# Performance work log

Measured on AMD Instinct MI355X. Metric: run time of the kernel, lower is better.

Reference implementation:

```python
import jax, jax.numpy as jnp
import numpy as np
import math

FEATURE_DIM = 1024
NUM_HEADS = 16
HEAD_SIZE = FEATURE_DIM // NUM_HEADS


def setup_inputs() -> dict:
    key = jax.random.key(0)
    ks = jax.random.split(key, 5)
    B, T, C = 4, 2048, FEATURE_DIM
    scale = 1.0 / math.sqrt(C)
    x = jax.random.normal(ks[0], (B, T, C), dtype=jnp.float32)
    # attention_proj: Linear(C, 3C) -> weight (3C, C), bias (3C,)
    W_qkv = jax.random.uniform(ks[1], (3 * C, C), jnp.float32, -scale, scale)
    b_qkv = jax.random.uniform(ks[2], (3 * C,), jnp.float32, -scale, scale)
    # final_proj: Linear(C, C)
    W_out = jax.random.uniform(ks[3], (C, C), jnp.float32, -scale, scale)
    b_out = jax.random.uniform(ks[4], (C,), jnp.float32, -scale, scale)
    return {"x": x, "W_qkv": W_qkv, "b_qkv": b_qkv, "W_out": W_out, "b_out": b_out}


def reference(x, W_qkv, b_qkv, W_out, b_out):
    B, T, C = x.shape
    H, hs = NUM_HEADS, HEAD_SIZE
    qkv = x @ W_qkv.T + b_qkv                     # (B, T, 3C)
    qkv = qkv.reshape(B, T, H, 3 * hs)            # per-head interleaved q|k|v
    q = qkv[..., :hs]                             # (B, T, H, hs)
    k = qkv[..., hs:2 * hs]
    v = qkv[..., 2 * hs:]
    att = jnp.einsum('bthd,bshd->bhts', q, k) / math.sqrt(hs)  # (B, H, T, T)
    att_prob = jax.nn.softmax(att, axis=-1)
    att_v = jnp.einsum('bhts,bshd->bthd', att_prob, v)         # (B, T, H, hs)
    att_v = att_v.reshape(B, T, C)
    return att_v @ W_out.T + b_out
```

## Files before the change

### kernel.cpp

```cpp
#include <hip/hip_runtime.h>
#include <hip/hip_bf16.h>


typedef unsigned short u16;
typedef short bf16x8 __attribute__((ext_vector_type(8)));
typedef float floatx4 __attribute__((ext_vector_type(4)));

#define BB 4
#define TT 2048
#define CC 1024
#define HH 16
#define CEXP 0.18033688f

#if __has_builtin(__builtin_amdgcn_exp2f)
#define EXP2(x) __builtin_amdgcn_exp2f(x)
#else
#define EXP2(x) exp2f(x)
#endif

__device__ __forceinline__ u16 f2bf(float f) {
    __hip_bfloat16 h = __float2bfloat16(f);
    u16 r; __builtin_memcpy(&r, &h, 2); return r;
}
__device__ __forceinline__ unsigned pkbf(float lo, float hi) {
    __hip_bfloat162 h2 = __float22bfloat162_rn(float2{lo, hi});
    unsigned r; __builtin_memcpy(&r, &h2, 4); return r;
}
__device__ __forceinline__ bf16x8 cvt8(const float* p) {
    floatx4 a = *(const floatx4*)p;
    floatx4 b = *(const floatx4*)(p + 4);
    bf16x8 r;
    r[0] = (short)f2bf(a[0]); r[1] = (short)f2bf(a[1]);
    r[2] = (short)f2bf(a[2]); r[3] = (short)f2bf(a[3]);
    r[4] = (short)f2bf(b[0]); r[5] = (short)f2bf(b[1]);
    r[6] = (short)f2bf(b[2]); r[7] = (short)f2bf(b[3]);
    return r;
}
__device__ __forceinline__ int sw8(int row, int slot) {
    return row * 64 + (((slot ^ (row & 7)) & 7) << 3);
}
__device__ __forceinline__ void gll16(const u16* g, u16* l) {
    __builtin_amdgcn_global_load_lds(
        (const __attribute__((address_space(1))) unsigned*)g,
        (__attribute__((address_space(3))) unsigned*)l, 16, 0, 0);
}

__device__ __forceinline__ void pl32swap(unsigned& a, unsigned& b) {
#if __has_builtin(__builtin_amdgcn_permlane32_swap)
    typedef unsigned u32x2 __attribute__((ext_vector_type(2)));
    u32x2 r = __builtin_amdgcn_permlane32_swap(a, b, false, false);
    a = r[0]; b = r[1];
#else
    const bool up = (threadIdx.x & 32) != 0;
    unsigned as = (unsigned)__shfl_xor((int)a, 32);
    unsigned bs = (unsigned)__shfl_xor((int)b, 32);
    unsigned na = up ? bs : a;
    unsigned nb = up ? b : as;
    a = na; b = nb;
#endif
}
__device__ __forceinline__ void pl16swap(unsigned& a, unsigned& b) {
#if __has_builtin(__builtin_amdgcn_permlane16_swap)
    typedef unsigned u32x2 __attribute__((ext_vector_type(2)));
    u32x2 r = __builtin_amdgcn_permlane16_swap(a, b, false, false);
    a = r[0]; b = r[1];
#else
    const bool up = (threadIdx.x & 16) != 0;
    unsigned as = (unsigned)__shfl_xor((int)a, 16);
    unsigned bs = (unsigned)__shfl_xor((int)b, 16);
    unsigned na = up ? bs : a;
    unsigned nb = up ? b : as;
    a = na; b = nb;
#endif
}

__global__ __launch_bounds__(256) void cvt_all(const float* __restrict__ x,
                                               const float* __restrict__ wq,
                                               const float* __restrict__ wo,
                                               u16* __restrict__ xb,
                                               u16* __restrict__ wqb,
                                               u16* __restrict__ wob) {
    const int nx8 = 8388608 / 8, nq8 = 3145728 / 8, no8 = 1048576 / 8;
    const int n8 = nx8 + nq8 + no8;
    for (int i = blockIdx.x * blockDim.x + threadIdx.x; i < n8;
         i += gridDim.x * blockDim.x) {
        const float* src;
        u16* dst;
        if (i < nx8)            { src = x  + (size_t)i * 8;          dst = xb  + (size_t)i * 8; }
        else if (i < nx8 + nq8) { size_t j = i - nx8; src = wq + j * 8; dst = wqb + j * 8; }
        else                    { size_t j = i - nx8 - nq8; src = wo + j * 8; dst = wob + j * 8; }
        floatx4 a = *(const floatx4*)src;
        floatx4 b = *(const floatx4*)(src + 4);
        union { bf16x8 v; unsigned u[4]; } r;
        r.u[0] = pkbf(a[0], a[1]); r.u[1] = pkbf(a[2], a[3]);
        r.u[2] = pkbf(b[0], b[1]); r.u[3] = pkbf(b[2], b[3]);
        *(bf16x8*)dst = r.v;
    }
}

template <int SCATTER, int QSLOT>
__global__ __launch_bounds__(256) void gemm_lds(const u16* __restrict__ Ab,
                                                const u16* __restrict__ Bb,
                                                const float* __restrict__ bias,
                                                void* __restrict__ Cv,
                                                int K, int N) {
    __shared__ u16 As[128 * 64];
    __shared__ u16 Bs[128 * 64];

    const int tid  = threadIdx.x;
    const int lane = tid & 63;
    const int wave = tid >> 6;
    const int quad = lane >> 4;
    const int l15  = lane & 15;
    const int wm   = (wave >> 1) * 64;
    const int wn   = (wave & 1) * 64;
    const int blockM = blockIdx.y * 128;
    const int blockN = blockIdx.x * 128;

    floatx4 acc[4][4];
#pragma unroll
    for (int i = 0; i < 4; i++)
#pragma unroll
        for (int j = 0; j < 4; j++) acc[i][j] = (floatx4){0.f, 0.f, 0.f, 0.f};

    const int lr = lane >> 3;
    const int scol = ((lane & 7) ^ (lr & 7)) * 8;

    for (int k0 = 0; k0 < K; k0 += 64) {
        __syncthreads();
#pragma unroll
        for (int i = 0; i < 4; i++) {
            const int c = wave * 4 + i;
            const int row = blockM + c * 8 + lr;
            const u16* src;
            if (QSLOT) {
                const int b = row >> 11, t = row & 2047, h = k0 >> 6;
                src = Ab + ((size_t)((b * HH + h) * TT + t)) * 192 + scol;
            } else {
                src = Ab + (size_t)row * K + k0 + scol;
            }
            gll16(src, &As[c * 512]);
        }
#pragma unroll
        for (int i = 0; i < 4; i++) {
            const int c = wave * 4 + i;
            const int row = blockN + c * 8 + lr;
            gll16(Bb + (size_t)row * K + k0 + scol, &Bs[c * 512]);
        }
        __syncthreads();

#pragma unroll
        for (int ks = 0; ks < 2; ks++) {
            const int slot = ks * 4 + quad;
            bf16x8 af[4], bfr[4];
#pragma unroll
            for (int mi = 0; mi < 4; mi++)
                af[mi] = *(const bf16x8*)&As[sw8(wm + mi * 16 + l15, slot)];
#pragma unroll
            for (int ni = 0; ni < 4; ni++)
                bfr[ni] = *(const bf16x8*)&Bs[sw8(wn + ni * 16 + l15, slot)];
#pragma unroll
            for (int mi = 0; mi < 4; mi++)
#pragma unroll
                for (int ni = 0; ni < 4; ni++)
                    acc[mi][ni] = __builtin_amdgcn_mfma_f32_16x16x32_bf16(
                        af[mi], bfr[ni], acc[mi][ni], 0, 0, 0);
        }
    }

#pragma unroll
    for (int ni = 0; ni < 4; ni++) {
        const int col = blockN + wn + ni * 16 + l15;
        const float bv = bias[col];
        if (SCATTER) {
            const int h = col / 192;
            const int r = col - h * 192;
            const float qs = (r < 64) ? CEXP : 1.0f;
            u16* C = (u16*)Cv;
#pragma unroll
            for (int mi = 0; mi < 4; mi++)
#pragma unroll
                for (int reg = 0; reg < 4; reg++) {
                    const int row = blockM + wm + mi * 16 + quad * 4 + reg;
                    const int b = row >> 11, t = row & 2047;
                    C[((size_t)((b * HH + h) * TT + t)) * 192 + r] =
                        f2bf((acc[mi][ni][reg] + bv) * qs);
                }
        } else {
            float* C = (float*)Cv;
#pragma unroll
            for (int mi = 0; mi < 4; mi++)
#pragma unroll
                for (int reg = 0; reg < 4; reg++) {
                    const int row = blockM + wm + mi * 16 + quad * 4 + reg;
                    C[(size_t)row * N + col] = acc[mi][ni][reg] + bv;
                }
        }
    }
}

template <int SCATTER, int QSLOT>
__global__ __launch_bounds__(256) void gemm_bt(const void* __restrict__ Av,
                                               const float* __restrict__ Bw,
                                               const float* __restrict__ bias,
                                               void* __restrict__ Cv,
                                               int K, int N) {
    __shared__ u16 As[128 * 64];
    __shared__ u16 Bs[128 * 64];

    const int tid  = threadIdx.x;
    const int lane = tid & 63;
    const int wave = tid >> 6;
    const int quad = lane >> 4;
    const int l15  = lane & 15;
    const int wm   = (wave >> 1) * 64;
    const int wn   = (wave & 1) * 64;
    const int blockM = blockIdx.y * 128;
    const int blockN = blockIdx.x * 128;

    floatx4 acc[4][4];
#pragma unroll
    for (int i = 0; i < 4; i++)
#pragma unroll
        for (int j = 0; j < 4; j++) acc[i][j] = (floatx4){0.f, 0.f, 0.f, 0.f};

    const int srow = lane >> 3;
    const int scol = (lane & 7) * 8;

    for (int k0 = 0; k0 < K; k0 += 64) {
        bf16x8 at[4], bt[4];
#pragma unroll
        for (int i = 0; i < 4; i++) {
            const int row = blockM + (i * 4 + wave) * 8 + srow;
            if (QSLOT) {
                const int b = row >> 11, t = row & 2047, h = k0 >> 6;
                at[i] = *(const bf16x8*)((const u16*)Av
                         + ((size_t)((b * HH + h) * TT + t)) * 192 + scol);
            } else {
                at[i] = cvt8((const float*)Av + (size_t)row * K + k0 + scol);
            }
        }
#pragma unroll
        for (int i = 0; i < 4; i++)
            bt[i] = cvt8(Bw + (size_t)(blockN + (i * 4 + wave) * 8 + srow) * K + k0 + scol);

        __syncthreads();
#pragma unroll
        for (int i = 0; i < 4; i++)
            *(bf16x8*)&As[sw8((i * 4 + wave) * 8 + srow, lane & 7)] = at[i];
#pragma unroll
        for (int i = 0; i < 4; i++)
            *(bf16x8*)&Bs[sw8((i * 4 + wave) * 8 + srow, lane & 7)] = bt[i];
        __syncthreads();

#pragma unroll
        for (int ks = 0; ks < 2; ks++) {
            const int slot = ks * 4 + quad;
            bf16x8 af[4], bfr[4];
#pragma unroll
            for (int mi = 0; mi < 4; mi++)
                af[mi] = *(const bf16x8*)&As[sw8(wm + mi * 16 + l15, slot)];
#pragma unroll
            for (int ni = 0; ni < 4; ni++)
                bfr[ni] = *(const bf16x8*)&Bs[sw8(wn + ni * 16 + l15, slot)];
#pragma unroll
            for (int mi = 0; mi < 4; mi++)
#pragma unroll
                for (int ni = 0; ni < 4; ni++)
                    acc[mi][ni] = __builtin_amdgcn_mfma_f32_16x16x32_bf16(
                        af[mi], bfr[ni], acc[mi][ni], 0, 0, 0);
        }
    }

#pragma unroll
    for (int ni = 0; ni < 4; ni++) {
        const int col = blockN + wn + ni * 16 + l15;
        const float bv = bias[col];
        if (SCATTER) {
            const int h = col / 192;
            const int r = col - h * 192;
            const float qs = (r < 64) ? CEXP : 1.0f;
            u16* C = (u16*)Cv;
#pragma unroll
            for (int mi = 0; mi < 4; mi++)
#pragma unroll
                for (int reg = 0; reg < 4; reg++) {
                    const int row = blockM + wm + mi * 16 + quad * 4 + reg;
                    const int b = row >> 11, t = row & 2047;
                    C[((size_t)((b * HH + h) * TT + t)) * 192 + r] =
                        f2bf((acc[mi][ni][reg] + bv) * qs);
                }
        } else {
            float* C = (float*)Cv;
#pragma unroll
            for (int mi = 0; mi < 4; mi++)
#pragma unroll
                for (int reg = 0; reg < 4; reg++) {
                    const int row = blockM + wm + mi * 16 + quad * 4 + reg;
                    C[(size_t)row * N + col] = acc[mi][ni][reg] + bv;
                }
        }
    }
}

__global__ __launch_bounds__(256) void attn_fwd(u16* __restrict__ qkv) {
    __shared__ u16 Ks[64 * 64];
    __shared__ u16 Vts[64 * 64];

    const int tid  = threadIdx.x;
    const int lane = tid & 63;
    const int wave = tid >> 6;
    const int quad = lane >> 4;
    const int l15  = lane & 15;

    const int bh = blockIdx.y;
    const int t0 = blockIdx.x * 128;
    u16* Qg = qkv + (size_t)bh * TT * 192;

    bf16x8 qf[2][2];
#pragma unroll
    for (int qi = 0; qi < 2; qi++) {
        const int trow = t0 + wave * 32 + qi * 16 + l15;
#pragma unroll
        for (int ks = 0; ks < 2; ks++)
            qf[qi][ks] = *(const bf16x8*)(Qg + (size_t)trow * 192 + ks * 32 + quad * 8);
    }

    bf16x8 ones;
#pragma unroll
    for (int j = 0; j < 8; j++) ones[j] = (short)0x3F80;

    floatx4 o[2][4];
#pragma unroll
    for (int qi = 0; qi < 2; qi++)
#pragma unroll
        for (int di = 0; di < 4; di++) o[qi][di] = (floatx4){0.f, 0.f, 0.f, 0.f};
    floatx4 l_acc[2] = {(floatx4){0.f,0.f,0.f,0.f}, (floatx4){0.f,0.f,0.f,0.f}};

    const int lr = lane >> 3;
    const int scolsw = ((lane & 7) ^ (lr & 7)) * 8;
    const int vs   = lane;
    const int vd0  = wave * 16;

    for (int s0 = 0; s0 < TT; s0 += 64) {
        const u16* vp = Qg + (size_t)(s0 + vs) * 192 + 128 + vd0;
        bf16x8 v0 = *(const bf16x8*)vp;
        bf16x8 v1 = *(const bf16x8*)(vp + 8);

        __syncthreads();
#pragma unroll
        for (int i = 0; i < 2; i++) {
            const int c = wave * 2 + i;
            gll16(Qg + (size_t)(s0 + c * 8 + lr) * 192 + 64 + scolsw, &Ks[c * 512]);
        }
        {
            const int vslot = vs >> 3, voff = vs & 7;
#pragma unroll
            for (int j = 0; j < 8; j++) {
                const int row = vd0 + j;
                Vts[row * 64 + (((vslot ^ (row & 7)) & 7) << 3) + voff] = (u16)v0[j];
            }
#pragma unroll
            for (int j = 0; j < 8; j++) {
                const int row = vd0 + 8 + j;
                Vts[row * 64 + (((vslot ^ (row & 7)) & 7) << 3) + voff] = (u16)v1[j];
            }
        }
        __syncthreads();

        floatx4 s_acc[4][2];
#pragma unroll
        for (int si = 0; si < 4; si++)
#pragma unroll
            for (int qi = 0; qi < 2; qi++) s_acc[si][qi] = (floatx4){0.f, 0.f, 0.f, 0.f};
#pragma unroll
        for (int ks = 0; ks < 2; ks++) {
            const int slot = ks * 4 + quad;
            bf16x8 kf[4];
#pragma unroll
            for (int si = 0; si < 4; si++)
                kf[si] = *(const bf16x8*)&Ks[sw8(si * 16 + l15, slot)];
#pragma unroll
            for (int si = 0; si < 4; si++)
#pragma unroll
                for (int qi = 0; qi < 2; qi++)
                    s_acc[si][qi] = __builtin_amdgcn_mfma_f32_16x16x32_bf16(
                        kf[si], qf[qi][ks], s_acc[si][qi], 0, 0, 0);
        }

        unsigned c[4][2][2];
#pragma unroll
        for (int si = 0; si < 4; si++)
#pragma unroll
            for (int qi = 0; qi < 2; qi++) {
                floatx4 p;
#pragma unroll
                for (int r = 0; r < 4; r++) p[r] = EXP2(s_acc[si][qi][r]);
                c[si][qi][0] = pkbf(p[0], p[1]);
                c[si][qi][1] = pkbf(p[2], p[3]);
            }

        union PF { bf16x8 v; unsigned u[4]; } pf[2][2];
#pragma unroll
        for (int qi = 0; qi < 2; qi++)
#pragma unroll
            for (int ks = 0; ks < 2; ks++)
#pragma unroll
                for (int h = 0; h < 2; h++) {
                    unsigned a = c[2 * ks][qi][h];
                    unsigned b = c[2 * ks + 1][qi][h];
                    pl32swap(a, b);
                    pl16swap(a, b);
                    pf[qi][ks].u[h]     = a;
                    pf[qi][ks].u[2 + h] = b;
                }

#pragma unroll
        for (int ks = 0; ks < 2; ks++) {
            const int slot = ks * 4 + quad;
            bf16x8 vf[4];
#pragma unroll
            for (int di = 0; di < 4; di++)
                vf[di] = *(const bf16x8*)&Vts[sw8(di * 16 + l15, slot)];
#pragma unroll
            for (int qi = 0; qi < 2; qi++) {
#pragma unroll
                for (int di = 0; di < 4; di++)
                    o[qi][di] = __builtin_amdgcn_mfma_f32_16x16x32_bf16(
                        pf[qi][ks].v, vf[di], o[qi][di], 0, 0, 0);
                l_acc[qi] = __builtin_amdgcn_mfma_f32_16x16x32_bf16(
                    pf[qi][ks].v, ones, l_acc[qi], 0, 0, 0);
            }
        }
    }

#pragma unroll
    for (int qi = 0; qi < 2; qi++)
#pragma unroll
        for (int reg = 0; reg < 4; reg++) {
            const float inv_l = 1.0f / l_acc[qi][reg];
            const int trow = t0 + wave * 32 + qi * 16 + quad * 4 + reg;
#pragma unroll
            for (int di = 0; di < 4; di++)
                Qg[(size_t)trow * 192 + di * 16 + l15] = f2bf(o[qi][di][reg] * inv_l);
        }
}

extern "C" void kernel_launch(void* const* d_in, const int* in_sizes, int n_in,
                              void* d_out, int out_size, void* d_ws, size_t ws_size,
                              hipStream_t stream) {
    (void)out_size;
    float* out = (float*)d_out;

    const float *x = nullptr, *wq = nullptr, *bq = nullptr, *wo = nullptr, *bo = nullptr;
    int found = 0;
    for (int i = 0; i < n_in && i < 8; i++) {
        switch (in_sizes[i]) {
            case 8388608: x  = (const float*)d_in[i]; found |= 1;  break;
            case 3145728: wq = (const float*)d_in[i]; found |= 2;  break;
            case 3072:    bq = (const float*)d_in[i]; found |= 4;  break;
            case 1048576: wo = (const float*)d_in[i]; found |= 8;  break;
            case 1024:    bo = (const float*)d_in[i]; found |= 16; break;
        }
    }
    if (found != 31) {
        x  = (const float*)d_in[0]; wq = (const float*)d_in[1];
        bq = (const float*)d_in[2]; wo = (const float*)d_in[3];
        bo = (const float*)d_in[4];
    }

    u16* qkv = (u16*)d_ws;

    const dim3 g1(3 * CC / 128, BB * TT / 128), ga(TT / 128, BB * HH),
               g3(CC / 128, BB * TT / 128);

    if (ws_size >= 75497472u) {
        u16* xb  = qkv + 25165824;
        u16* wqb = qkv + 33554432;
        u16* wob = qkv + 36700160;
        cvt_all<<<2048, 256, 0, stream>>>(x, wq, wo, xb, wqb, wob);
        gemm_lds<1, 0><<<g1, 256, 0, stream>>>(xb, wqb, bq, qkv, CC, 3 * CC);
        attn_fwd<<<ga, 256, 0, stream>>>(qkv);
        gemm_lds<0, 1><<<g3, 256, 0, stream>>>(qkv, wob, bo, out, CC, CC);
    } else {
        gemm_bt<1, 0><<<g1, 256, 0, stream>>>(x, wq, bq, qkv, CC, 3 * CC);
        attn_fwd<<<ga, 256, 0, stream>>>(qkv);
        gemm_bt<0, 1><<<g3, 256, 0, stream>>>(qkv, wo, bo, out, CC, CC);
    }
}
```

Before: 295.0 us.

## Split attention block across eight waves with one query tile each and MFMA priority

The attention kernel now launches 512 threads per block, so eight waves each own 16 query rows instead of four waves owning 32. K/V tile loading is redistributed so each thread stages 8 V values and one K chunk. s_setprio hints are placed around the MFMA sections. The goal is more waves per CU to hide latency, at the cost of halving MFMA work per shared K/V tile load per wave and adding more barrier participants.

```diff
diff --git a/kernel.cpp b/kernel.cpp
--- a/kernel.cpp
+++ b/kernel.cpp
@@ -303,7 +303,7 @@
     }
 }
 
-__global__ __launch_bounds__(256) void attn_fwd(u16* __restrict__ qkv) {
+__global__ __launch_bounds__(512) void attn_fwd(u16* __restrict__ qkv) {
     __shared__ u16 Ks[64 * 64];
     __shared__ u16 Vts[64 * 64];
 
@@ -317,42 +317,34 @@
     const int t0 = blockIdx.x * 128;
     u16* Qg = qkv + (size_t)bh * TT * 192;
 
-    bf16x8 qf[2][2];
-#pragma unroll
-    for (int qi = 0; qi < 2; qi++) {
-        const int trow = t0 + wave * 32 + qi * 16 + l15;
+    bf16x8 qf[2];
+    {
+        const int trow = t0 + wave * 16 + l15;
 #pragma unroll
         for (int ks = 0; ks < 2; ks++)
-            qf[qi][ks] = *(const bf16x8*)(Qg + (size_t)trow * 192 + ks * 32 + quad * 8);
+            qf[ks] = *(const bf16x8*)(Qg + (size_t)trow * 192 + ks * 32 + quad * 8);
     }
 
     bf16x8 ones;
 #pragma unroll
     for (int j = 0; j < 8; j++) ones[j] = (short)0x3F80;
 
-    floatx4 o[2][4];
-#pragma unroll
-    for (int qi = 0; qi < 2; qi++)
-#pragma unroll
-        for (int di = 0; di < 4; di++) o[qi][di] = (floatx4){0.f, 0.f, 0.f, 0.f};
-    floatx4 l_acc[2] = {(floatx4){0.f,0.f,0.f,0.f}, (floatx4){0.f,0.f,0.f,0.f}};
+    floatx4 o[4];
+#pragma unroll
+    for (int di = 0; di < 4; di++) o[di] = (floatx4){0.f, 0.f, 0.f, 0.f};
+    floatx4 l_acc = (floatx4){0.f, 0.f, 0.f, 0.f};
 
     const int lr = lane >> 3;
     const int scolsw = ((lane & 7) ^ (lr & 7)) * 8;
-    const int vs   = lane;
-    const int vd0  = wave * 16;
+    const int vs  = tid & 63;
+    const int vd0 = (tid >> 6) * 8;
 
     for (int s0 = 0; s0 < TT; s0 += 64) {
-        const u16* vp = Qg + (size_t)(s0 + vs) * 192 + 128 + vd0;
-        bf16x8 v0 = *(const bf16x8*)vp;
-        bf16x8 v1 = *(const bf16x8*)(vp + 8);
-
-        __syncthreads();
-#pragma unroll
-        for (int i = 0; i < 2; i++) {
-            const int c = wave * 2 + i;
-            gll16(Qg + (size_t)(s0 + c * 8 + lr) * 192 + 64 + scolsw, &Ks[c * 512]);
-        }
+        bf16x8 v0 = *(const bf16x8*)(Qg + (size_t)(s0 + vs) * 192 + 128 + vd0);
+
+        __syncthreads();
+        gll16(Qg + (size_t)(s0 + wave * 8 + lr) * 192 + 64 + scolsw,
+              &Ks[wave * 512]);
         {
             const int vslot = vs >> 3, voff = vs & 7;
 #pragma unroll
@@ -360,19 +352,13 @@
                 const int row = vd0 + j;
                 Vts[row * 64 + (((vslot ^ (row & 7)) & 7) << 3) + voff] = (u16)v0[j];
             }
-#pragma unroll
-            for (int j = 0; j < 8; j++) {
-                const int row = vd0 + 8 + j;
-                Vts[row * 64 + (((vslot ^ (row & 7)) & 7) << 3) + voff] = (u16)v1[j];
-            }
-        }
-        __syncthreads();
-
-        floatx4 s_acc[4][2];
-#pragma unroll
-        for (int si = 0; si < 4; si++)
-#pragma unroll
-            for (int qi = 0; qi < 2; qi++) s_acc[si][qi] = (floatx4){0.f, 0.f, 0.f, 0.f};
+        }
+        __syncthreads();
+
+        floatx4 s_acc[4];
+#pragma unroll
+        for (int si = 0; si < 4; si++) s_acc[si] = (floatx4){0.f, 0.f, 0.f, 0.f};
+        __builtin_amdgcn_s_setprio(1);
 #pragma unroll
         for (int ks = 0; ks < 2; ks++) {
             const int slot = ks * 4 + quad;
@@ -382,39 +368,35 @@
                 kf[si] = *(const bf16x8*)&Ks[sw8(si * 16 + l15, slot)];
 #pragma unroll
             for (int si = 0; si < 4; si++)
-#pragma unroll
-                for (int qi = 0; qi < 2; qi++)
-                    s_acc[si][qi] = __builtin_amdgcn_mfma_f32_16x16x32_bf16(
-                        kf[si], qf[qi][ks], s_acc[si][qi], 0, 0, 0);
-        }
-
-        unsigned c[4][2][2];
-#pragma unroll
-        for (int si = 0; si < 4; si++)
-#pragma unroll
-            for (int qi = 0; qi < 2; qi++) {
-                floatx4 p;
-#pragma unroll
-                for (int r = 0; r < 4; r++) p[r] = EXP2(s_acc[si][qi][r]);
-                c[si][qi][0] = pkbf(p[0], p[1]);
-                c[si][qi][1] = pkbf(p[2], p[3]);
+                s_acc[si] = __builtin_amdgcn_mfma_f32_16x16x32_bf16(
+                    kf[si], qf[ks], s_acc[si], 0, 0, 0);
+        }
+        __builtin_amdgcn_s_setprio(0);
+
+        unsigned c[4][2];
+#pragma unroll
+        for (int si = 0; si < 4; si++) {
+            floatx4 p;
+#pragma unroll
+            for (int r = 0; r < 4; r++) p[r] = EXP2(s_acc[si][r]);
+            c[si][0] = pkbf(p[0], p[1]);
+            c[si][1] = pkbf(p[2], p[3]);
+        }
+
+        union PF { bf16x8 v; unsigned u[4]; } pf[2];
+#pragma unroll
+        for (int ks = 0; ks < 2; ks++)
+#pragma unroll
+            for (int h = 0; h < 2; h++) {
+                unsigned a = c[2 * ks][h];
+                unsigned b = c[2 * ks + 1][h];
+                pl32swap(a, b);
+                pl16swap(a, b);
+                pf[ks].u[h]     = a;
+                pf[ks].u[2 + h] = b;
             }
 
-        union PF { bf16x8 v; unsigned u[4]; } pf[2][2];
-#pragma unroll
-        for (int qi = 0; qi < 2; qi++)
-#pragma unroll
-            for (int ks = 0; ks < 2; ks++)
-#pragma unroll
-                for (int h = 0; h < 2; h++) {
-                    unsigned a = c[2 * ks][qi][h];
-                    unsigned b = c[2 * ks + 1][qi][h];
-                    pl32swap(a, b);
-                    pl16swap(a, b);
-                    pf[qi][ks].u[h]     = a;
-                    pf[qi][ks].u[2 + h] = b;
-                }
-
+        __builtin_amdgcn_s_setprio(1);
 #pragma unroll
         for (int ks = 0; ks < 2; ks++) {
             const int slot = ks * 4 + quad;
@@ -423,27 +405,23 @@
             for (int di = 0; di < 4; di++)
                 vf[di] = *(const bf16x8*)&Vts[sw8(di * 16 + l15, slot)];
 #pragma unroll
-            for (int qi = 0; qi < 2; qi++) {
-#pragma unroll
-                for (int di = 0; di < 4; di++)
-                    o[qi][di] = __builtin_amdgcn_mfma_f32_16x16x32_bf16(
-                        pf[qi][ks].v, vf[di], o[qi][di], 0, 0, 0);
-                l_acc[qi] = __builtin_amdgcn_mfma_f32_16x16x32_bf16(
-                    pf[qi][ks].v, ones, l_acc[qi], 0, 0, 0);
-            }
-        }
-    }
-
-#pragma unroll
-    for (int qi = 0; qi < 2; qi++)
-#pragma unroll
-        for (int reg = 0; reg < 4; reg++) {
-            const float inv_l = 1.0f / l_acc[qi][reg];
-            const int trow = t0 + wave * 32 + qi * 16 + quad * 4 + reg;
-#pragma unroll
             for (int di = 0; di < 4; di++)
-                Qg[(size_t)trow * 192 + di * 16 + l15] = f2bf(o[qi][di][reg] * inv_l);
-        }
+                o[di] = __builtin_amdgcn_mfma_f32_16x16x32_bf16(
+                    pf[ks].v, vf[di], o[di], 0, 0, 0);
+            l_acc = __builtin_amdgcn_mfma_f32_16x16x32_bf16(
+                pf[ks].v, ones, l_acc, 0, 0, 0);
+        }
+        __builtin_amdgcn_s_setprio(0);
+    }
+
+#pragma unroll
+    for (int reg = 0; reg < 4; reg++) {
+        const float inv_l = 1.0f / l_acc[reg];
+        const int trow = t0 + wave * 16 + quad * 4 + reg;
+#pragma unroll
+        for (int di = 0; di < 4; di++)
+            Qg[(size_t)trow * 192 + di * 16 + l15] = f2bf(o[di][reg] * inv_l);
+    }
 }
 
 extern "C" void kernel_launch(void* const* d_in, const int* in_sizes, int n_in,
@@ -480,11 +458,11 @@
         u16* wob = qkv + 36700160;
         cvt_all<<<2048, 256, 0, stream>>>(x, wq, wo, xb, wqb, wob);
         gemm_lds<1, 0><<<g1, 256, 0, stream>>>(xb, wqb, bq, qkv, CC, 3 * CC);
-        attn_fwd<<<ga, 256, 0, stream>>>(qkv);
+        attn_fwd<<<ga, 512, 0, stream>>>(qkv);
         gemm_lds<0, 1><<<g3, 256, 0, stream>>>(qkv, wob, bo, out, CC, CC);
     } else {
         gemm_bt<1, 0><<<g1, 256, 0, stream>>>(x, wq, bq, qkv, CC, 3 * CC);
-        attn_fwd<<<ga, 256, 0, stream>>>(qkv);
+        attn_fwd<<<ga, 512, 0, stream>>>(qkv);
         gemm_bt<0, 1><<<g3, 256, 0, stream>>>(qkv, wo, bo, out, CC, CC);
     }
 }
```

Measured after the change: 287.7 us. -2.5%, faster.
